# Kernel optimization log

Hardware: AMD Instinct MI355X
Metric: run time of the kernel (lower is better)

## Reference

```python
import jax, jax.numpy as jnp
import numpy as np

DECAY = 0.9    # LIF membrane decay
THRESH = 1.0   # firing threshold


def spike(x):
    # Heaviside spike (forward only)
    return (x > 0).astype(x.dtype)


def setup_inputs() -> dict:
    key = jax.random.key(0)
    k0, k1, k2, k3, k4 = jax.random.split(key, 5)
    B, D, H, O = 4096, 256, 512, 2
    x = jax.random.normal(k0, (B, D), dtype=jnp.float32)
    # torch.nn.Linear-style scaled init
    W1 = jax.random.normal(k1, (H, D), dtype=jnp.float32) * (1.0 / np.sqrt(D))
    b1 = jax.random.normal(k2, (H,), dtype=jnp.float32) * (1.0 / np.sqrt(D))
    W2 = jax.random.normal(k3, (O, H), dtype=jnp.float32) * (1.0 / np.sqrt(H))
    b2 = jax.random.normal(k4, (O,), dtype=jnp.float32) * (1.0 / np.sqrt(H))
    return {"x": x, "W1": W1, "b1": b1, "W2": W2, "b2": b2, "time_steps": 100}


def reference(x, W1, b1, W2, b2, time_steps):
    # Input is identical at every timestep, so fc1 can be hoisted out of the loop.
    h1 = x @ W1.T + b1                         # [B, H]
    B = x.shape[0]
    O = W2.shape[0]

    def step(carry, _):
        mem1, out_spikes = carry
        mem1 = DECAY * mem1 + h1               # leaky integrate
        s1 = spike(mem1 - THRESH)              # fire
        mem1 = mem1 - s1 * THRESH              # soft reset
        h2 = s1 @ W2.T + b2                    # [B, O]
        s2 = spike(h2)
        return (mem1, out_spikes + s2), None

    init = (jnp.zeros_like(h1), jnp.zeros((B, O), dtype=x.dtype))
    (mem1, out_spikes), _ = jax.lax.scan(step, init, None, length=time_steps)
    return out_spikes / time_steps
```

## Files before the change

### kernel.cpp

```cpp
#include <hip/hip_runtime.h>


template <int CTRL>
__device__ __forceinline__ float dpp_add(float v) {
    int x = __builtin_amdgcn_update_dpp(0, __builtin_bit_cast(int, v),
                                        CTRL, 0xF, 0xF, false);
    return v + __builtin_bit_cast(float, x);
}

__device__ __forceinline__ float swz_xor16_add(float v) {
    int x = __builtin_amdgcn_ds_swizzle(__builtin_bit_cast(int, v), 0x401F);
    return v + __builtin_bit_cast(float, x);
}

#define TM 64
#define TN 64
#define XS_STRIDE4 17
#define WS_STRIDE  68

__global__ __launch_bounds__(512)
__attribute__((amdgpu_waves_per_eu(4, 4)))
void snn_fc1_kernel(const float* __restrict__ x,
                    const float* __restrict__ W1,
                    const float* __restrict__ b1,
                    float* __restrict__ h1ws)
{
    __shared__ float4 xs4[TM * XS_STRIDE4];
    __shared__ float  wsf[64 * WS_STRIDE];

    const int tid  = threadIdx.x;
    const int row0 = blockIdx.x * TM;
    const int col0 = blockIdx.y * TN;

    const int tx = tid & 15;
    const int ty = tid >> 4;

    float acc[2][4];
    {
        const float4 bv = ((const float4*)b1)[(col0 >> 2) + tx];
        #pragma unroll
        for (int r = 0; r < 2; ++r) {
            acc[r][0] = bv.x; acc[r][1] = bv.y;
            acc[r][2] = bv.z; acc[r][3] = bv.w;
        }
    }

    const float4* xg = (const float4*)x;
    const float4* wg = (const float4*)W1;

    for (int chunk = 0; chunk < 4; ++chunk) {
        const int k0q = chunk * 16;

        #pragma unroll
        for (int i = 0; i < 2; ++i) {
            const int idx = tid + i * 512;
            const int row = idx >> 4;
            const int q   = idx & 15;
            xs4[row * XS_STRIDE4 + q] =
                xg[(size_t)(row0 + row) * 64 + k0q + q];
        }
        #pragma unroll
        for (int i = 0; i < 2; ++i) {
            const int idx = tid + i * 512;
            const int q   = idx & 15;
            const int c   = idx >> 4;
            const float4 wv4 = wg[(size_t)(col0 + c) * 64 + k0q + q];
            wsf[(q * 4 + 0) * WS_STRIDE + c] = wv4.x;
            wsf[(q * 4 + 1) * WS_STRIDE + c] = wv4.y;
            wsf[(q * 4 + 2) * WS_STRIDE + c] = wv4.z;
            wsf[(q * 4 + 3) * WS_STRIDE + c] = wv4.w;
        }
        __syncthreads();

        #pragma unroll
        for (int k4 = 0; k4 < 16; ++k4) {
            float4 xv[2], wv[4];
            #pragma unroll
            for (int r = 0; r < 2; ++r)
                xv[r] = xs4[(ty * 2 + r) * XS_STRIDE4 + k4];
            #pragma unroll
            for (int kk = 0; kk < 4; ++kk)
                wv[kk] = *(const float4*)&wsf[(k4 * 4 + kk) * WS_STRIDE + tx * 4];
            #pragma unroll
            for (int kk = 0; kk < 4; ++kk) {
                const float xk0 = xv[0][kk], xk1 = xv[1][kk];
                #pragma unroll
                for (int cc = 0; cc < 4; ++cc) {
                    const float w = wv[kk][cc];
                    acc[0][cc] = fmaf(xk0, w, acc[0][cc]);
                    acc[1][cc] = fmaf(xk1, w, acc[1][cc]);
                }
            }
        }
        __syncthreads();
    }

    #pragma unroll
    for (int r = 0; r < 2; ++r) {
        float4* dst = (float4*)&h1ws[(size_t)(row0 + ty * 2 + r) * 512
                                     + col0 + tx * 4];
        *dst = make_float4(acc[r][0], acc[r][1], acc[r][2], acc[r][3]);
    }
}

#define DEAD_CUT 0.0999f
#define TB 10

template <int E>
__device__ __forceinline__ void lif_body4(const float* __restrict__ ch,
                                          const float* __restrict__ cw0,
                                          const float* __restrict__ cw1,
                                          int l31, bool lo16, float bbl,
                                          int T, float* __restrict__ dst)
{
    float hv[E], w0r[E], w1r[E], mem[E];
    #pragma unroll
    for (int j = 0; j < E; ++j) {
        hv[j]  = ch [j * 32 + l31];
        w0r[j] = cw0[j * 32 + l31];
        w1r[j] = cw1[j * 32 + l31];
        mem[j] = 0.0f;
    }
    unsigned cnt = 0;
    int t = 0;

    for (; t + TB <= T; t += TB) {
        float d[TB];
        #pragma unroll
        for (int k = 0; k < TB; ++k) {
            float a0 = 0.0f, a1 = 0.0f, a0b = 0.0f, a1b = 0.0f;
            #pragma unroll
            for (int j = 0; j < E; ++j) {
                const float m = __fadd_rn(__fmul_rn(0.9f, mem[j]), hv[j]);
                const float s = (m > 1.0f) ? 1.0f : 0.0f;
                mem[j] = m - s;
                if ((j & 1) == 0) { a0  = fmaf(s, w0r[j], a0);  a1  = fmaf(s, w1r[j], a1);  }
                else              { a0b = fmaf(s, w0r[j], a0b); a1b = fmaf(s, w1r[j], a1b); }
            }
            a0 += a0b; a1 += a1b;
            const float b = swz_xor16_add(a0);
            const float c = swz_xor16_add(a1);
            d[k] = lo16 ? b : c;
        }
        #pragma unroll
        for (int k = 0; k < TB; ++k) d[k] = dpp_add<0x121>(d[k]);
        #pragma unroll
        for (int k = 0; k < TB; ++k) d[k] = dpp_add<0x122>(d[k]);
        #pragma unroll
        for (int k = 0; k < TB; ++k) d[k] = dpp_add<0x124>(d[k]);
        #pragma unroll
        for (int k = 0; k < TB; ++k) d[k] = dpp_add<0x128>(d[k]);
        #pragma unroll
        for (int k = 0; k < TB; ++k)
            cnt += (__fadd_rn(d[k], bbl) > 0.0f) ? 1u : 0u;
    }

    for (; t < T; ++t) {
        float a0 = 0.0f, a1 = 0.0f, a0b = 0.0f, a1b = 0.0f;
        #pragma unroll
        for (int j = 0; j < E; ++j) {
            const float m = __fadd_rn(__fmul_rn(0.9f, mem[j]), hv[j]);
            const float s = (m > 1.0f) ? 1.0f : 0.0f;
            mem[j] = m - s;
            if ((j & 1) == 0) { a0  = fmaf(s, w0r[j], a0);  a1  = fmaf(s, w1r[j], a1);  }
            else              { a0b = fmaf(s, w0r[j], a0b); a1b = fmaf(s, w1r[j], a1b); }
        }
        a0 += a0b; a1 += a1b;
        const float b = swz_xor16_add(a0);
        const float c = swz_xor16_add(a1);
        float e = lo16 ? b : c;
        e = dpp_add<0x121>(e);
        e = dpp_add<0x122>(e);
        e = dpp_add<0x124>(e);
        e = dpp_add<0x128>(e);
        cnt += (__fadd_rn(e, bbl) > 0.0f) ? 1u : 0u;
    }

    const int other = __builtin_amdgcn_ds_swizzle((int)cnt, 0x401F);
    if (l31 == 0) {
        const float ft = (float)T;
        *(float2*)dst = make_float2((float)cnt / ft, (float)other / ft);
    }
}

__global__ __launch_bounds__(256)
__attribute__((amdgpu_waves_per_eu(2, 4)))
void snn_lif_kernel(const float* __restrict__ h1ws,
                    const float* __restrict__ W2,
                    const float* __restrict__ b2,
                    const int* __restrict__ tsp,
                    float* __restrict__ out)
{
    __shared__ float ch [8][512];
    __shared__ float cw0[8][512];
    __shared__ float cw1[8][512];

    const int tid  = threadIdx.x;
    const int l    = tid & 63;
    const int wid  = tid >> 6;
    const int half = l >> 5;
    const int l31  = l & 31;
    const int rowA = blockIdx.x * 8 + wid * 2;

    unsigned bases[2];
    #pragma unroll
    for (int r = 0; r < 2; ++r) {
        const int cr = wid * 2 + r;
        #pragma unroll
        for (int j = 0; j < 8; ++j) {
            ch [cr][j * 64 + l] = 0.0f;
            cw0[cr][j * 64 + l] = 0.0f;
            cw1[cr][j * 64 + l] = 0.0f;
        }
        const float* hrow = h1ws + (size_t)(rowA + r) * 512;
        unsigned base = 0;
        #pragma unroll
        for (int j = 0; j < 8; ++j) {
            const int h = j * 64 + l;
            const float v  = hrow[h];
            const float w0 = W2[h];
            const float w1 = W2[512 + h];
            const bool live = v > DEAD_CUT;
            const unsigned long long m = __ballot(live);
            const unsigned pos = base + (unsigned)__popcll(m & ((1ull << l) - 1ull));
            if (live && pos < 512u) {
                ch [cr][pos] = v;
                cw0[cr][pos] = w0;
                cw1[cr][pos] = w1;
            }
            base += (unsigned)__popcll(m);
        }
        bases[r] = base;
    }

    const float bb0 = b2[0], bb1 = b2[1];
    const int   T   = tsp[0];
    const int   row = rowA + half;
    float* dst = out + (size_t)row * 2;
    const bool  lo16 = (l31 < 16);
    const float bbl  = lo16 ? bb0 : bb1;

    const unsigned mx = bases[0] > bases[1] ? bases[0] : bases[1];
    int trips = (int)((mx + 31u) >> 5);
    if (trips < 1)  trips = 1;
    if (trips > 10) trips = 10;
    const float* chp  = ch [wid * 2 + half];
    const float* cw0p = cw0[wid * 2 + half];
    const float* cw1p = cw1[wid * 2 + half];

    switch (trips) {
        case 1:  lif_body4<1> (chp, cw0p, cw1p, l31, lo16, bbl, T, dst); break;
        case 2:  lif_body4<2> (chp, cw0p, cw1p, l31, lo16, bbl, T, dst); break;
        case 3:  lif_body4<3> (chp, cw0p, cw1p, l31, lo16, bbl, T, dst); break;
        case 4:  lif_body4<4> (chp, cw0p, cw1p, l31, lo16, bbl, T, dst); break;
        case 5:  lif_body4<5> (chp, cw0p, cw1p, l31, lo16, bbl, T, dst); break;
        case 6:  lif_body4<6> (chp, cw0p, cw1p, l31, lo16, bbl, T, dst); break;
        case 7:  lif_body4<7> (chp, cw0p, cw1p, l31, lo16, bbl, T, dst); break;
        case 8:  lif_body4<8> (chp, cw0p, cw1p, l31, lo16, bbl, T, dst); break;
        case 9:  lif_body4<9> (chp, cw0p, cw1p, l31, lo16, bbl, T, dst); break;
        default: lif_body4<10>(chp, cw0p, cw1p, l31, lo16, bbl, T, dst); break;
    }
}

#define BM 16
#define LDS_H_STRIDE 520

__global__ __launch_bounds__(256, 1) void snn_fused_kernel(
    const float* __restrict__ x, const float* __restrict__ W1,
    const float* __restrict__ b1, const float* __restrict__ W2,
    const float* __restrict__ b2, const int* __restrict__ tsp,
    float* __restrict__ out)
{
    __shared__ float xs[BM * 256];
    __shared__ float h1s[BM * LDS_H_STRIDE];

    const int tid  = threadIdx.x;
    const int row0 = blockIdx.x * BM;

    {
        const float4* xg  = (const float4*)(x + (size_t)row0 * 256);
        float4*       xsv = (float4*)xs;
        #pragma unroll
        for (int i = 0; i < 4; ++i)
            xsv[i * 256 + tid] = xg[i * 256 + tid];
    }
    __syncthreads();

    {
        const int h0 = tid * 2;
        float acc0[BM], acc1[BM];
        const float bia0 = b1[h0], bia1 = b1[h0 + 1];
        #pragma unroll
        for (int b = 0; b < BM; ++b) { acc0[b] = bia0; acc1[b] = bia1; }
        const float4* w0v = (const float4*)(W1 + (size_t)h0 * 256);
        const float4* w1v = (const float4*)(W1 + (size_t)(h0 + 1) * 256);
        const float4* xsv = (const float4*)xs;
        float4 wa = w0v[0], wb = w1v[0];
        #pragma unroll 1
        for (int k4 = 0; k4 < 64; ++k4) {
            const int kn = (k4 < 63) ? k4 + 1 : 63;
            float4 wan = w0v[kn], wbn = w1v[kn];
            float4 xv[BM];
            #pragma unroll
            for (int b = 0; b < BM; ++b) xv[b] = xsv[b * 64 + k4];
            #pragma unroll
            for (int b = 0; b < BM; ++b) {
                acc0[b] = fmaf(xv[b].x, wa.x, acc0[b]);
                acc0[b] = fmaf(xv[b].y, wa.y, acc0[b]);
                acc0[b] = fmaf(xv[b].z, wa.z, acc0[b]);
                acc0[b] = fmaf(xv[b].w, wa.w, acc0[b]);
                acc1[b] = fmaf(xv[b].x, wb.x, acc1[b]);
                acc1[b] = fmaf(xv[b].y, wb.y, acc1[b]);
                acc1[b] = fmaf(xv[b].z, wb.z, acc1[b]);
                acc1[b] = fmaf(xv[b].w, wb.w, acc1[b]);
            }
            wa = wan; wb = wbn;
        }
        #pragma unroll
        for (int b = 0; b < BM; ++b) {
            float2* dst = (float2*)&h1s[b * LDS_H_STRIDE + h0];
            *dst = make_float2(acc0[b], acc1[b]);
        }
    }
    __syncthreads();

    {
        const int l   = tid & 63;
        const int w   = tid >> 6;
        const int l15 = l & 15;
        const int b_local = w * 4 + (l >> 4);
        const int row = row0 + b_local;

        float hv[32], w0r[32], w1r[32], mem[32];
        #pragma unroll
        for (int j = 0; j < 32; ++j) {
            const int h = l15 + j * 16;
            hv[j]  = h1s[b_local * LDS_H_STRIDE + h];
            w0r[j] = W2[h];
            w1r[j] = W2[512 + h];
            mem[j] = 0.0f;
        }
        const float bb0 = b2[0], bb1 = b2[1];
        const int   T   = tsp[0];

        float c0 = 0.0f, c1 = 0.0f;
        for (int t = 0; t < T; ++t) {
            float a0 = 0.0f, a1 = 0.0f, a0b = 0.0f, a1b = 0.0f;
            #pragma unroll
            for (int j = 0; j < 32; j += 2) {
                float m0 = __fadd_rn(__fmul_rn(0.9f, mem[j]),     hv[j]);
                float m1 = __fadd_rn(__fmul_rn(0.9f, mem[j + 1]), hv[j + 1]);
                float s0 = (m0 > 1.0f) ? 1.0f : 0.0f;
                float s1 = (m1 > 1.0f) ? 1.0f : 0.0f;
                mem[j]     = m0 - s0;
                mem[j + 1] = m1 - s1;
                a0  = fmaf(s0, w0r[j],     a0);
                a1  = fmaf(s0, w1r[j],     a1);
                a0b = fmaf(s1, w0r[j + 1], a0b);
                a1b = fmaf(s1, w1r[j + 1], a1b);
            }
            a0 += a0b; a1 += a1b;
            a0 = dpp_add<0x121>(a0); a1 = dpp_add<0x121>(a1);
            a0 = dpp_add<0x122>(a0); a1 = dpp_add<0x122>(a1);
            a0 = dpp_add<0x124>(a0); a1 = dpp_add<0x124>(a1);
            a0 = dpp_add<0x128>(a0); a1 = dpp_add<0x128>(a1);
            c0 += ((a0 + bb0) > 0.0f) ? 1.0f : 0.0f;
            c1 += ((a1 + bb1) > 0.0f) ? 1.0f : 0.0f;
        }

        if (l15 == 0) {
            const float ft = (float)T;
            float2* dst = (float2*)(out + (size_t)row * 2);
            *dst = make_float2(c0 / ft, c1 / ft);
        }
    }
}

extern "C" void kernel_launch(void* const* d_in, const int* in_sizes, int n_in,
                              void* d_out, int out_size, void* d_ws, size_t ws_size,
                              hipStream_t stream) {
    const float* x   = (const float*)d_in[0];
    const float* W1  = (const float*)d_in[1];
    const float* b1  = (const float*)d_in[2];
    const float* W2  = (const float*)d_in[3];
    const float* b2  = (const float*)d_in[4];
    const int*   tsp = (const int*)d_in[5];
    float*       out = (float*)d_out;

    const int B = in_sizes[0] / 256;
    const size_t need = (size_t)B * 512 * sizeof(float);

    if (ws_size >= need) {
        float* h1ws = (float*)d_ws;
        snn_fc1_kernel<<<dim3(B / TM, 512 / TN), dim3(512), 0, stream>>>(
            x, W1, b1, h1ws);
        snn_lif_kernel<<<dim3(B / 8), dim3(256), 0, stream>>>(
            h1ws, W2, b2, tsp, out);
    } else {
        snn_fused_kernel<<<dim3(B / BM), dim3(256), 0, stream>>>(
            x, W1, b1, W2, b2, tsp, out);
    }
}
```

Before: 61.18 us.

## Fuse fc1 GEMM and compacted LIF loop into a single kernel

Drops the separate tiled fc1 kernel and its global h1 workspace round-trip. The fused kernel computes a block of 8 rows of h1 into LDS, then runs the dead-neuron compaction and the templated LIF body on that LDS data in the same block. This removes one launch and the global write and read of h1. In exchange, the fc1 GEMM now uses a simple per-block scheme with little reuse of W1: each 8-row block reads all of W1. LDS use per block also grows, which may limit occupancy.

```diff
diff --git a/kernel.cpp b/kernel.cpp
--- a/kernel.cpp
+++ b/kernel.cpp
@@ -1,5 +1,10 @@
 #include <hip/hip_runtime.h>
 
+
+#define BM 8
+#define H_STRIDE 520
+#define DEAD_CUT 0.0999f
+#define TB 10
 
 template <int CTRL>
 __device__ __forceinline__ float dpp_add(float v) {
@@ -12,99 +17,6 @@
     int x = __builtin_amdgcn_ds_swizzle(__builtin_bit_cast(int, v), 0x401F);
     return v + __builtin_bit_cast(float, x);
 }
-
-#define TM 64
-#define TN 64
-#define XS_STRIDE4 17
-#define WS_STRIDE  68
-
-__global__ __launch_bounds__(512)
-__attribute__((amdgpu_waves_per_eu(4, 4)))
-void snn_fc1_kernel(const float* __restrict__ x,
-                    const float* __restrict__ W1,
-                    const float* __restrict__ b1,
-                    float* __restrict__ h1ws)
-{
-    __shared__ float4 xs4[TM * XS_STRIDE4];
-    __shared__ float  wsf[64 * WS_STRIDE];
-
-    const int tid  = threadIdx.x;
-    const int row0 = blockIdx.x * TM;
-    const int col0 = blockIdx.y * TN;
-
-    const int tx = tid & 15;
-    const int ty = tid >> 4;
-
-    float acc[2][4];
-    {
-        const float4 bv = ((const float4*)b1)[(col0 >> 2) + tx];
-        #pragma unroll
-        for (int r = 0; r < 2; ++r) {
-            acc[r][0] = bv.x; acc[r][1] = bv.y;
-            acc[r][2] = bv.z; acc[r][3] = bv.w;
-        }
-    }
-
-    const float4* xg = (const float4*)x;
-    const float4* wg = (const float4*)W1;
-
-    for (int chunk = 0; chunk < 4; ++chunk) {
-        const int k0q = chunk * 16;
-
-        #pragma unroll
-        for (int i = 0; i < 2; ++i) {
-            const int idx = tid + i * 512;
-            const int row = idx >> 4;
-            const int q   = idx & 15;
-            xs4[row * XS_STRIDE4 + q] =
-                xg[(size_t)(row0 + row) * 64 + k0q + q];
-        }
-        #pragma unroll
-        for (int i = 0; i < 2; ++i) {
-            const int idx = tid + i * 512;
-            const int q   = idx & 15;
-            const int c   = idx >> 4;
-            const float4 wv4 = wg[(size_t)(col0 + c) * 64 + k0q + q];
-            wsf[(q * 4 + 0) * WS_STRIDE + c] = wv4.x;
-            wsf[(q * 4 + 1) * WS_STRIDE + c] = wv4.y;
-            wsf[(q * 4 + 2) * WS_STRIDE + c] = wv4.z;
-            wsf[(q * 4 + 3) * WS_STRIDE + c] = wv4.w;
-        }
-        __syncthreads();
-
-        #pragma unroll
-        for (int k4 = 0; k4 < 16; ++k4) {
-            float4 xv[2], wv[4];
-            #pragma unroll
-            for (int r = 0; r < 2; ++r)
-                xv[r] = xs4[(ty * 2 + r) * XS_STRIDE4 + k4];
-            #pragma unroll
-            for (int kk = 0; kk < 4; ++kk)
-                wv[kk] = *(const float4*)&wsf[(k4 * 4 + kk) * WS_STRIDE + tx * 4];
-            #pragma unroll
-            for (int kk = 0; kk < 4; ++kk) {
-                const float xk0 = xv[0][kk], xk1 = xv[1][kk];
-                #pragma unroll
-                for (int cc = 0; cc < 4; ++cc) {
-                    const float w = wv[kk][cc];
-                    acc[0][cc] = fmaf(xk0, w, acc[0][cc]);
-                    acc[1][cc] = fmaf(xk1, w, acc[1][cc]);
-                }
-            }
-        }
-        __syncthreads();
-    }
-
-    #pragma unroll
-    for (int r = 0; r < 2; ++r) {
-        float4* dst = (float4*)&h1ws[(size_t)(row0 + ty * 2 + r) * 512
-                                     + col0 + tx * 4];
-        *dst = make_float4(acc[r][0], acc[r][1], acc[r][2], acc[r][3]);
-    }
-}
-
-#define DEAD_CUT 0.0999f
-#define TB 10
 
 template <int E>
 __device__ __forceinline__ void lif_body4(const float* __restrict__ ch,
@@ -185,94 +97,19 @@
 
 __global__ __launch_bounds__(256)
 __attribute__((amdgpu_waves_per_eu(2, 4)))
-void snn_lif_kernel(const float* __restrict__ h1ws,
-                    const float* __restrict__ W2,
-                    const float* __restrict__ b2,
-                    const int* __restrict__ tsp,
-                    float* __restrict__ out)
+void snn_fused_kernel(const float* __restrict__ x,
+                      const float* __restrict__ W1,
+                      const float* __restrict__ b1,
+                      const float* __restrict__ W2,
+                      const float* __restrict__ b2,
+                      const int* __restrict__ tsp,
+                      float* __restrict__ out)
 {
-    __shared__ float ch [8][512];
-    __shared__ float cw0[8][512];
-    __shared__ float cw1[8][512];
-
-    const int tid  = threadIdx.x;
-    const int l    = tid & 63;
-    const int wid  = tid >> 6;
-    const int half = l >> 5;
-    const int l31  = l & 31;
-    const int rowA = blockIdx.x * 8 + wid * 2;
-
-    unsigned bases[2];
-    #pragma unroll
-    for (int r = 0; r < 2; ++r) {
-        const int cr = wid * 2 + r;
-        #pragma unroll
-        for (int j = 0; j < 8; ++j) {
-            ch [cr][j * 64 + l] = 0.0f;
-            cw0[cr][j * 64 + l] = 0.0f;
-            cw1[cr][j * 64 + l] = 0.0f;
-        }
-        const float* hrow = h1ws + (size_t)(rowA + r) * 512;
-        unsigned base = 0;
-        #pragma unroll
-        for (int j = 0; j < 8; ++j) {
-            const int h = j * 64 + l;
-            const float v  = hrow[h];
-            const float w0 = W2[h];
-            const float w1 = W2[512 + h];
-            const bool live = v > DEAD_CUT;
-            const unsigned long long m = __ballot(live);
-            const unsigned pos = base + (unsigned)__popcll(m & ((1ull << l) - 1ull));
-            if (live && pos < 512u) {
-                ch [cr][pos] = v;
-                cw0[cr][pos] = w0;
-                cw1[cr][pos] = w1;
-            }
-            base += (unsigned)__popcll(m);
-        }
-        bases[r] = base;
-    }
-
-    const float bb0 = b2[0], bb1 = b2[1];
-    const int   T   = tsp[0];
-    const int   row = rowA + half;
-    float* dst = out + (size_t)row * 2;
-    const bool  lo16 = (l31 < 16);
-    const float bbl  = lo16 ? bb0 : bb1;
-
-    const unsigned mx = bases[0] > bases[1] ? bases[0] : bases[1];
-    int trips = (int)((mx + 31u) >> 5);
-    if (trips < 1)  trips = 1;
-    if (trips > 10) trips = 10;
-    const float* chp  = ch [wid * 2 + half];
-    const float* cw0p = cw0[wid * 2 + half];
-    const float* cw1p = cw1[wid * 2 + half];
-
-    switch (trips) {
-        case 1:  lif_body4<1> (chp, cw0p, cw1p, l31, lo16, bbl, T, dst); break;
-        case 2:  lif_body4<2> (chp, cw0p, cw1p, l31, lo16, bbl, T, dst); break;
-        case 3:  lif_body4<3> (chp, cw0p, cw1p, l31, lo16, bbl, T, dst); break;
-        case 4:  lif_body4<4> (chp, cw0p, cw1p, l31, lo16, bbl, T, dst); break;
-        case 5:  lif_body4<5> (chp, cw0p, cw1p, l31, lo16, bbl, T, dst); break;
-        case 6:  lif_body4<6> (chp, cw0p, cw1p, l31, lo16, bbl, T, dst); break;
-        case 7:  lif_body4<7> (chp, cw0p, cw1p, l31, lo16, bbl, T, dst); break;
-        case 8:  lif_body4<8> (chp, cw0p, cw1p, l31, lo16, bbl, T, dst); break;
-        case 9:  lif_body4<9> (chp, cw0p, cw1p, l31, lo16, bbl, T, dst); break;
-        default: lif_body4<10>(chp, cw0p, cw1p, l31, lo16, bbl, T, dst); break;
-    }
-}
-
-#define BM 16
-#define LDS_H_STRIDE 520
-
-__global__ __launch_bounds__(256, 1) void snn_fused_kernel(
-    const float* __restrict__ x, const float* __restrict__ W1,
-    const float* __restrict__ b1, const float* __restrict__ W2,
-    const float* __restrict__ b2, const int* __restrict__ tsp,
-    float* __restrict__ out)
-{
-    __shared__ float xs[BM * 256];
-    __shared__ float h1s[BM * LDS_H_STRIDE];
+    __shared__ float xs [BM * 256];
+    __shared__ float h1s[BM * H_STRIDE];
+    __shared__ float ch [BM][512];
+    __shared__ float cw0[BM][512];
+    __shared__ float cw1[BM][512];
 
     const int tid  = threadIdx.x;
     const int row0 = blockIdx.x * BM;
@@ -281,7 +118,7 @@
         const float4* xg  = (const float4*)(x + (size_t)row0 * 256);
         float4*       xsv = (float4*)xs;
         #pragma unroll
-        for (int i = 0; i < 4; ++i)
+        for (int i = 0; i < 2; ++i)
             xsv[i * 256 + tid] = xg[i * 256 + tid];
     }
     __syncthreads();
@@ -292,9 +129,11 @@
         const float bia0 = b1[h0], bia1 = b1[h0 + 1];
         #pragma unroll
         for (int b = 0; b < BM; ++b) { acc0[b] = bia0; acc1[b] = bia1; }
+
         const float4* w0v = (const float4*)(W1 + (size_t)h0 * 256);
         const float4* w1v = (const float4*)(W1 + (size_t)(h0 + 1) * 256);
         const float4* xsv = (const float4*)xs;
+
         float4 wa = w0v[0], wb = w1v[0];
         #pragma unroll 1
         for (int k4 = 0; k4 < 64; ++k4) {
@@ -318,60 +157,76 @@
         }
         #pragma unroll
         for (int b = 0; b < BM; ++b) {
-            float2* dst = (float2*)&h1s[b * LDS_H_STRIDE + h0];
+            float2* dst = (float2*)&h1s[b * H_STRIDE + h0];
             *dst = make_float2(acc0[b], acc1[b]);
         }
     }
     __syncthreads();
 
     {
-        const int l   = tid & 63;
-        const int w   = tid >> 6;
-        const int l15 = l & 15;
-        const int b_local = w * 4 + (l >> 4);
-        const int row = row0 + b_local;
-
-        float hv[32], w0r[32], w1r[32], mem[32];
-        #pragma unroll
-        for (int j = 0; j < 32; ++j) {
-            const int h = l15 + j * 16;
-            hv[j]  = h1s[b_local * LDS_H_STRIDE + h];
-            w0r[j] = W2[h];
-            w1r[j] = W2[512 + h];
-            mem[j] = 0.0f;
-        }
+        const int l    = tid & 63;
+        const int wid  = tid >> 6;
+        const int half = l >> 5;
+        const int l31  = l & 31;
+        const int rA   = wid * 2;
+
+        unsigned bases[2];
+        #pragma unroll
+        for (int r = 0; r < 2; ++r) {
+            const int cr = rA + r;
+            #pragma unroll
+            for (int j = 0; j < 8; ++j) {
+                ch [cr][j * 64 + l] = 0.0f;
+                cw0[cr][j * 64 + l] = 0.0f;
+                cw1[cr][j * 64 + l] = 0.0f;
+            }
+            const float* hrow = &h1s[(size_t)cr * H_STRIDE];
+            unsigned base = 0;
+            #pragma unroll
+            for (int j = 0; j < 8; ++j) {
+                const int h = j * 64 + l;
+                const float v  = hrow[h];
+                const float w0 = W2[h];
+                const float w1 = W2[512 + h];
+                const bool live = v > DEAD_CUT;
+                const unsigned long long m = __ballot(live);
+                const unsigned pos = base + (unsigned)__popcll(m & ((1ull << l) - 1ull));
+                if (live && pos < 512u) {
+                    ch [cr][pos] = v;
+                    cw0[cr][pos] = w0;
+                    cw1[cr][pos] = w1;
+                }
+                base += (unsigned)__popcll(m);
+            }
+            bases[r] = base;
+        }
+
         const float bb0 = b2[0], bb1 = b2[1];
         const int   T   = tsp[0];
-
-        float c0 = 0.0f, c1 = 0.0f;
-        for (int t = 0; t < T; ++t) {
-            float a0 = 0.0f, a1 = 0.0f, a0b = 0.0f, a1b = 0.0f;
-            #pragma unroll
-            for (int j = 0; j < 32; j += 2) {
-                float m0 = __fadd_rn(__fmul_rn(0.9f, mem[j]),     hv[j]);
-                float m1 = __fadd_rn(__fmul_rn(0.9f, mem[j + 1]), hv[j + 1]);
-                float s0 = (m0 > 1.0f) ? 1.0f : 0.0f;
-                float s1 = (m1 > 1.0f) ? 1.0f : 0.0f;
-                mem[j]     = m0 - s0;
-                mem[j + 1] = m1 - s1;
-                a0  = fmaf(s0, w0r[j],     a0);
-                a1  = fmaf(s0, w1r[j],     a1);
-                a0b = fmaf(s1, w0r[j + 1], a0b);
-                a1b = fmaf(s1, w1r[j + 1], a1b);
-            }
-            a0 += a0b; a1 += a1b;
-            a0 = dpp_add<0x121>(a0); a1 = dpp_add<0x121>(a1);
-            a0 = dpp_add<0x122>(a0); a1 = dpp_add<0x122>(a1);
-            a0 = dpp_add<0x124>(a0); a1 = dpp_add<0x124>(a1);
-            a0 = dpp_add<0x128>(a0); a1 = dpp_add<0x128>(a1);
-            c0 += ((a0 + bb0) > 0.0f) ? 1.0f : 0.0f;
-            c1 += ((a1 + bb1) > 0.0f) ? 1.0f : 0.0f;
-        }
-
-        if (l15 == 0) {
-            const float ft = (float)T;
-            float2* dst = (float2*)(out + (size_t)row * 2);
-            *dst = make_float2(c0 / ft, c1 / ft);
+        const int   row = row0 + rA + half;
+        float* dst = out + (size_t)row * 2;
+        const bool  lo16 = (l31 < 16);
+        const float bbl  = lo16 ? bb0 : bb1;
+
+        const unsigned mx = bases[0] > bases[1] ? bases[0] : bases[1];
+        int trips = (int)((mx + 31u) >> 5);
+        if (trips < 1)  trips = 1;
+        if (trips > 10) trips = 10;
+        const float* chp  = ch [rA + half];
+        const float* cw0p = cw0[rA + half];
+        const float* cw1p = cw1[rA + half];
+
+        switch (trips) {
+            case 1:  lif_body4<1> (chp, cw0p, cw1p, l31, lo16, bbl, T, dst); break;
+            case 2:  lif_body4<2> (chp, cw0p, cw1p, l31, lo16, bbl, T, dst); break;
+            case 3:  lif_body4<3> (chp, cw0p, cw1p, l31, lo16, bbl, T, dst); break;
+            case 4:  lif_body4<4> (chp, cw0p, cw1p, l31, lo16, bbl, T, dst); break;
+            case 5:  lif_body4<5> (chp, cw0p, cw1p, l31, lo16, bbl, T, dst); break;
+            case 6:  lif_body4<6> (chp, cw0p, cw1p, l31, lo16, bbl, T, dst); break;
+            case 7:  lif_body4<7> (chp, cw0p, cw1p, l31, lo16, bbl, T, dst); break;
+            case 8:  lif_body4<8> (chp, cw0p, cw1p, l31, lo16, bbl, T, dst); break;
+            case 9:  lif_body4<9> (chp, cw0p, cw1p, l31, lo16, bbl, T, dst); break;
+            default: lif_body4<10>(chp, cw0p, cw1p, l31, lo16, bbl, T, dst); break;
         }
     }
 }
@@ -388,16 +243,6 @@
     float*       out = (float*)d_out;
 
     const int B = in_sizes[0] / 256;
-    const size_t need = (size_t)B * 512 * sizeof(float);
-
-    if (ws_size >= need) {
-        float* h1ws = (float*)d_ws;
-        snn_fc1_kernel<<<dim3(B / TM, 512 / TN), dim3(512), 0, stream>>>(
-            x, W1, b1, h1ws);
-        snn_lif_kernel<<<dim3(B / 8), dim3(256), 0, stream>>>(
-            h1ws, W2, b2, tsp, out);
-    } else {
-        snn_fused_kernel<<<dim3(B / BM), dim3(256), 0, stream>>>(
-            x, W1, b1, W2, b2, tsp, out);
-    }
-}
+    snn_fused_kernel<<<dim3(B / BM), dim3(256), 0, stream>>>(
+        x, W1, b1, W2, b2, tsp, out);
+}
```

After: 85.23 us. +39.3%, slower.
